# Kernel tuning notes

Measured on AMD Instinct MI355X. Metric: run time of the kernel, lower is better.

## Reference

```python
import jax, jax.numpy as jnp
import numpy as np

VOCAB = 32000
EMBED = 512
HID = 1024          # bi-LSTM summary dim; each direction HID//2
HDIM = 1024         # snli_h_dim
B, T = 128, 128
EPS = 1e-6


def setup_inputs() -> dict:
    key = jax.random.key(0)
    ks = jax.random.split(key, 10)
    Hh = HID // 2
    def rn(k, shape, scale):
        return jax.random.normal(k, shape, jnp.float32) * scale
    embed = rn(ks[0], (VOCAB, EMBED), 0.1).at[0].set(0.0)  # padding_idx=0 row zeroed
    return {
        'hyp_tokens': jax.random.randint(ks[1], (B, T), 0, VOCAB),
        'prem_tokens': jax.random.randint(ks[2], (B, T), 0, VOCAB),
        'embed': embed,
        'W_ih': rn(ks[3], (4 * Hh, EMBED), 1.0 / np.sqrt(Hh)),
        'W_hh': rn(ks[4], (4 * Hh, Hh), 1.0 / np.sqrt(Hh)),
        'b_ih': jnp.zeros((4 * Hh,), jnp.float32),
        'b_hh': jnp.zeros((4 * Hh,), jnp.float32),
        'mlp1_W': rn(ks[5], (HDIM, 4 * HID), np.sqrt(2.0 / (4 * HID))),  # He init
        'mlp1_b': jnp.zeros((HDIM,), jnp.float32),
        'mlp2_W': rn(ks[6], (HDIM, HDIM), np.sqrt(2.0 / HDIM)),
        'mlp2_b': jnp.zeros((HDIM,), jnp.float32),
        'out_W': rn(ks[7], (3, HDIM), np.sqrt(2.0 / HDIM)),
        'out_b': jnp.zeros((3,), jnp.float32),
        'ln0_g': jnp.ones((4 * HID,), jnp.float32), 'ln0_b': jnp.zeros((4 * HID,), jnp.float32),
        'ln1_g': jnp.ones((HDIM,), jnp.float32), 'ln1_b': jnp.zeros((HDIM,), jnp.float32),
        'ln2_g': jnp.ones((HDIM,), jnp.float32), 'ln2_b': jnp.zeros((HDIM,), jnp.float32),
    }


def _lstm_final(x_tbe, W_ih, W_hh, b_ih, b_hh):
    # Runs an LSTM over time (leading axis), returns final (h, c).
    Bn = x_tbe.shape[1]
    Hh = W_hh.shape[1]
    # Precompute input projection for all timesteps: [T, B, 4*Hh]
    xg = jnp.einsum('tbe,ge->tbg', x_tbe, W_ih) + b_ih + b_hh
    def step(carry, xg_t):
        h, c = carry
        gates = xg_t + h @ W_hh.T
        i, f, g, o = jnp.split(gates, 4, axis=-1)  # PyTorch gate order i,f,g,o
        c2 = jax.nn.sigmoid(f) * c + jax.nn.sigmoid(i) * jnp.tanh(g)
        h2 = jax.nn.sigmoid(o) * jnp.tanh(c2)
        return (h2, c2), None
    init = (jnp.zeros((Bn, Hh), x_tbe.dtype), jnp.zeros((Bn, Hh), x_tbe.dtype))
    (h, c), _ = jax.lax.scan(step, init, xg)
    return h, c


def _encode_sent(x, W_ih, W_hh, b_ih, b_hh):
    # Matches encode_sent: same LSTM weights run forward and backward over time;
    # summary = concat(last forward state, last backward state).
    xt = jnp.swapaxes(x, 0, 1)  # [T, B, E]
    hf, cf = _lstm_final(xt, W_ih, W_hh, b_ih, b_hh)
    hb, cb = _lstm_final(xt[::-1], W_ih, W_hh, b_ih, b_hh)
    return jnp.concatenate([hf, hb], axis=-1), jnp.concatenate([cf, cb], axis=-1)


def _ln(x, g, b):
    m = jnp.mean(x, axis=-1, keepdims=True)
    v = jnp.var(x, axis=-1, keepdims=True)
    return (x - m) * jax.lax.rsqrt(v + EPS) * g + b


def reference(hyp_tokens, prem_tokens, embed, W_ih, W_hh, b_ih, b_hh,
              mlp1_W, mlp1_b, mlp2_W, mlp2_b, out_W, out_b,
              ln0_g, ln0_b, ln1_g, ln1_b, ln2_g, ln2_b):
    hyp_e = embed[hyp_tokens]    # [B, T, E]
    prem_e = embed[prem_tokens]
    hyp_h, _ = _encode_sent(hyp_e, W_ih, W_hh, b_ih, b_hh)    # [B, HID]
    prem_h, _ = _encode_sent(prem_e, W_ih, W_hh, b_ih, b_hh)
    # prepare_features: [hyp, prem, prem - hyp, hyp * prem]
    f = jnp.concatenate([hyp_h, prem_h, prem_h - hyp_h, hyp_h * prem_h], axis=-1)
    f = _ln(f, ln0_g, ln0_b)
    f = jax.nn.relu(f @ mlp1_W.T + mlp1_b)
    f = _ln(f, ln1_g, ln1_b)
    f = jax.nn.relu(f @ mlp2_W.T + mlp2_b)
    f = _ln(f, ln2_g, ln2_b)
    return f @ out_W.T + out_b  # [B, 3] logits
```

## Files before the change

kernel.cpp:

```cpp
#include <hip/hip_runtime.h>
#include <hip/hip_bf16.h>

typedef __hip_bfloat16 bf16;
typedef __attribute__((ext_vector_type(8))) short short8;
typedef __attribute__((ext_vector_type(4))) short s16x4;
typedef __attribute__((ext_vector_type(4))) float f32x4;
typedef __attribute__((ext_vector_type(2))) float f32x2;

#define TB 128
#define TT 128
#define EMB 512
#define HH 512
#define G4 2048
#define NROWS 512
#define F4 4096
#define HD 1024

__device__ __forceinline__ bf16 f2bf(float x){ return __float2bfloat16(x); }
__device__ __forceinline__ float bf2f(bf16 x){ return __bfloat162float(x); }

__device__ __forceinline__ float fsigm(float x){
    return __builtin_amdgcn_rcpf(1.f + __builtin_amdgcn_exp2f(-1.44269504089f * x));
}
__device__ __forceinline__ float ftanh(float x){
    float t = __builtin_amdgcn_exp2f(2.88539008178f * x);
    return 1.f - 2.f * __builtin_amdgcn_rcpf(t + 1.f);
}

__device__ __forceinline__ short8 pack8(float4 a, float4 b){
    short8 r;
    r[0] = (short)__bfloat16_as_ushort(f2bf(a.x));
    r[1] = (short)__bfloat16_as_ushort(f2bf(a.y));
    r[2] = (short)__bfloat16_as_ushort(f2bf(a.z));
    r[3] = (short)__bfloat16_as_ushort(f2bf(a.w));
    r[4] = (short)__bfloat16_as_ushort(f2bf(b.x));
    r[5] = (short)__bfloat16_as_ushort(f2bf(b.y));
    r[6] = (short)__bfloat16_as_ushort(f2bf(b.z));
    r[7] = (short)__bfloat16_as_ushort(f2bf(b.w));
    return r;
}

__global__ __launch_bounds__(256) void k_cvt(const float* __restrict__ src,
                                             bf16* __restrict__ dst, int n4)
{
    for (int i = blockIdx.x * 256 + threadIdx.x; i < n4; i += gridDim.x * 256) {
        float4 v = reinterpret_cast<const float4*>(src)[i];
        s16x4 o;
        o[0] = (short)__bfloat16_as_ushort(f2bf(v.x));
        o[1] = (short)__bfloat16_as_ushort(f2bf(v.y));
        o[2] = (short)__bfloat16_as_ushort(f2bf(v.z));
        o[3] = (short)__bfloat16_as_ushort(f2bf(v.w));
        reinterpret_cast<s16x4*>(dst)[i] = o;
    }
}

__global__ __launch_bounds__(256) void k_gather(
    const int* __restrict__ tok_h, const int* __restrict__ tok_p,
    const float* __restrict__ embed, bf16* __restrict__ x_bf)
{
    const int total4 = 2 * TT * TB * (EMB / 4);
    for (int g = blockIdx.x * 256 + threadIdx.x; g < total4; g += gridDim.x * 256) {
        int e4 = g & (EMB / 4 - 1);
        int b  = (g >> 7) & 127;
        int t  = (g >> 14) & 127;
        int s  = g >> 21;
        int tok = (s ? tok_p : tok_h)[b * TT + t];
        float4 v = reinterpret_cast<const float4*>(embed + (size_t)tok * EMB)[e4];
        s16x4 o;
        o[0] = (short)__bfloat16_as_ushort(f2bf(v.x));
        o[1] = (short)__bfloat16_as_ushort(f2bf(v.y));
        o[2] = (short)__bfloat16_as_ushort(f2bf(v.z));
        o[3] = (short)__bfloat16_as_ushort(f2bf(v.w));
        reinterpret_cast<s16x4*>(x_bf + (((size_t)s * TT + t) * TB + b) * EMB)[e4] = o;
    }
}

__global__ __launch_bounds__(256) void k_xproj2(
    const int* __restrict__ tok_h, const int* __restrict__ tok_p,
    const float* __restrict__ embed, const bf16* __restrict__ W_ihb,
    const float* __restrict__ b_ih, const float* __restrict__ b_hh,
    bf16* __restrict__ xg)
{
    __shared__ __align__(16) short As[64][512];
    const int mb = blockIdx.x;
    const int nb = blockIdx.y;
    const int tid = threadIdx.x;
    const int w = tid >> 6, lane = tid & 63, l16 = lane & 15, kq = lane >> 4;
    const int m0 = mb * 64;
    const int s  = m0 >> 14;
    const int tt = (m0 >> 7) & 127;
    const int bbase = m0 & 127;
    const int* tp = s ? tok_p : tok_h;

#pragma unroll
    for (int it = 0; it < 16; ++it) {
        int idx = it * 256 + tid;
        int row = idx >> 6;
        int ch  = idx & 63;
        int tok = tp[(bbase + row) * TT + tt];
        const float* er = embed + (size_t)tok * EMB + ch * 8;
        float4 v0 = *(const float4*)er;
        float4 v1 = *(const float4*)(er + 4);
        *(short8*)&As[row][(ch ^ (row & 7)) * 8] = pack8(v0, v1);
    }
    __syncthreads();

    const int c0 = nb * 256 + w * 64;
    f32x4 acc[4][4];
#pragma unroll
    for (int mt = 0; mt < 4; ++mt)
#pragma unroll
        for (int nt = 0; nt < 4; ++nt) acc[mt][nt] = (f32x4)0.f;

    for (int kk = 0; kk < 16; ++kk) {
        short8 bfr[4];
#pragma unroll
        for (int nt = 0; nt < 4; ++nt)
            bfr[nt] = *(const short8*)(W_ihb + (size_t)(c0 + nt * 16 + l16) * EMB + kk * 32 + kq * 8);
#pragma unroll
        for (int mt = 0; mt < 4; ++mt) {
            int row = mt * 16 + l16;
            short8 a = *(const short8*)&As[row][(((kk * 4 + kq) ^ (row & 7)) * 8)];
#pragma unroll
            for (int nt = 0; nt < 4; ++nt)
                acc[mt][nt] = __builtin_amdgcn_mfma_f32_16x16x32_bf16(a, bfr[nt], acc[mt][nt], 0, 0, 0);
        }
    }
#pragma unroll
    for (int nt = 0; nt < 4; ++nt) {
        int col = c0 + nt * 16 + l16;
        float bias = b_ih[col] + b_hh[col];
#pragma unroll
        for (int mt = 0; mt < 4; ++mt)
#pragma unroll
            for (int q = 0; q < 4; ++q) {
                int m = m0 + mt * 16 + kq * 4 + q;
                xg[(size_t)m * G4 + col] = f2bf(acc[mt][nt][q] + bias);
            }
    }
}

__global__ __launch_bounds__(512, 1) void k_persist8(
    const bf16* __restrict__ xg, const float* __restrict__ W_hh,
    const float* __restrict__ b_ih, const float* __restrict__ b_hh,
    float* __restrict__ h_f32, float* __restrict__ h_fin,
    int* __restrict__ slots, int* __restrict__ xinfo)
{
    __shared__ __align__(16) short hstage[2][16][512];
    __shared__ float ga[16][16][18];

    const int tid = threadIdx.x;
    const int bid = blockIdx.x;
    const int rg = bid & 31;
    const int cb = bid >> 5;
    const int w = tid >> 6, lane = tid & 63, l16 = lane & 15, kq = lane >> 4;
    const int j0 = cb * 64;
    const int r0 = rg * 16;
    const int run = rg >> 3;
    const int s = run >> 1, dirb = run & 1;
    const int b0 = (rg & 7) * 16;

    bool mall = false;
    {
        int myx;
        asm volatile("s_getreg_b32 %0, hwreg(HW_REG_XCC_ID)" : "=s"(myx));
        if (tid == 0)
            __hip_atomic_store(&xinfo[bid], (myx & 15) + 1,
                               __ATOMIC_RELAXED, __HIP_MEMORY_SCOPE_AGENT);
        int v0 = 0;
        for (int c = 0; c < 8; ++c) {
            int v;
            do {
                v = __hip_atomic_load(&xinfo[c * 32 + rg],
                                      __ATOMIC_RELAXED, __HIP_MEMORY_SCOPE_AGENT);
                if (!v) __builtin_amdgcn_s_sleep(2);
            } while (!v);
            if (c == 0) v0 = v;
            else if (v != v0) mall = true;
        }
    }

    short8 Bf[2][16];
#pragma unroll
    for (int nt = 0; nt < 2; ++nt) {
        int n = 2 * w + nt;
        int gcol = (n >> 2) * HH + j0 + (n & 3) * 16 + l16;
        const float* wr = W_hh + (size_t)gcol * HH;
#pragma unroll
        for (int kk = 0; kk < 16; ++kk) {
            float4 v0 = *(const float4*)(wr + kk * 32 + kq * 8);
            float4 v1 = *(const float4*)(wr + kk * 32 + kq * 8 + 4);
            Bf[nt][kk] = pack8(v0, v1);
        }
    }

    const int urow = tid >> 5;
    const int jseg = tid & 31;
    float bsum[2][4];
#pragma unroll
    for (int e = 0; e < 2; ++e)
#pragma unroll
        for (int g = 0; g < 4; ++g) {
            int j = g * HH + j0 + jseg * 2 + e;
            bsum[e][g] = b_ih[j] + b_hh[j];
        }
    float creg[2] = {0.f, 0.f};
    const size_t HSF = (size_t)NROWS * HH;

    int rowoff[8];
#pragma unroll
    for (int nt = 0; nt < 2; ++nt) {
        int n = 2 * w + nt;
        int gcol = (n >> 2) * HH + j0 + (n & 3) * 16 + l16;
#pragma unroll
        for (int q = 0; q < 4; ++q)
            rowoff[nt * 4 + q] = (b0 + kq * 4 + q) * G4 + gcol;
    }

    unsigned xp[8];
    {
        int te0 = dirb ? (TT - 1) : 0;
        const bf16* xr = xg + ((size_t)(s * TT + te0) * TB) * G4;
#pragma unroll
        for (int i = 0; i < 8; ++i)
            xp[i] = (unsigned)__bfloat16_as_ushort(xr[rowoff[i]]);
    }

    for (int t = 0; t < TT; ++t) {
        const int p = t & 1;

        f32x4 hv[4];
        {
            unsigned long long a = (unsigned long long)(
                h_f32 + (size_t)p * HSF + (size_t)(r0 + urow) * HH + jseg * 16);
            if (mall) {
#pragma unroll
                for (int i = 0; i < 4; ++i)
                    asm volatile("global_load_dwordx4 %0, %1, off sc0 sc1"
                                 : "=v"(hv[i]) : "v"(a + i * 16));
            } else {
#pragma unroll
                for (int i = 0; i < 4; ++i)
                    asm volatile("global_load_dwordx4 %0, %1, off sc0"
                                 : "=v"(hv[i]) : "v"(a + i * 16));
            }
        }
        asm volatile("s_waitcnt vmcnt(0)" ::: "memory");
        __builtin_amdgcn_sched_barrier(0);

#pragma unroll
        for (int half = 0; half < 2; ++half) {
            short8 hi, lo;
#pragma unroll
            for (int i2 = 0; i2 < 8; ++i2) {
                float v = hv[half * 2 + (i2 >> 2)][i2 & 3];
                bf16 hb = f2bf(v);
                hi[i2] = (short)__bfloat16_as_ushort(hb);
                lo[i2] = (short)__bfloat16_as_ushort(f2bf(v - bf2f(hb)));
            }
            int ch = (2 * jseg + half) ^ (urow & 7);
            *(short8*)&hstage[0][urow][ch * 8] = hi;
            *(short8*)&hstage[1][urow][ch * 8] = lo;
        }

        f32x4 acc[2];
#pragma unroll
        for (int nt = 0; nt < 2; ++nt)
#pragma unroll
            for (int q = 0; q < 4; ++q)
                acc[nt][q] = __uint_as_float(xp[nt * 4 + q] << 16);

        __syncthreads();

#pragma unroll
        for (int kk = 0; kk < 16; ++kk) {
            int ch = ((kk * 4 + kq) ^ (l16 & 7)) * 8;
            short8 ahi = *(const short8*)&hstage[0][l16][ch];
            short8 alo = *(const short8*)&hstage[1][l16][ch];
#pragma unroll
            for (int nt = 0; nt < 2; ++nt) {
                acc[nt] = __builtin_amdgcn_mfma_f32_16x16x32_bf16(alo, Bf[nt][kk], acc[nt], 0, 0, 0);
                acc[nt] = __builtin_amdgcn_mfma_f32_16x16x32_bf16(ahi, Bf[nt][kk], acc[nt], 0, 0, 0);
            }
        }

#pragma unroll
        for (int nt = 0; nt < 2; ++nt)
#pragma unroll
            for (int q = 0; q < 4; ++q)
                ga[2 * w + nt][kq * 4 + q][l16] = acc[nt][q];
        __syncthreads();

        float hn2[2];
#pragma unroll
        for (int e = 0; e < 2; ++e) {
            int jc = jseg * 2 + e;
            int sub = jc >> 4, c15 = jc & 15;
            float pi = ga[0 + sub][urow][c15]  + bsum[e][0];
            float pf = ga[4 + sub][urow][c15]  + bsum[e][1];
            float pg = ga[8 + sub][urow][c15]  + bsum[e][2];
            float po = ga[12 + sub][urow][c15] + bsum[e][3];
            float cn = fsigm(pf) * creg[e] + fsigm(pi) * ftanh(pg);
            float hn = fsigm(po) * ftanh(cn);
            creg[e] = cn;
            hn2[e] = hn;
        }
        {
            unsigned long long a = (unsigned long long)(
                h_f32 + (size_t)(p ^ 1) * HSF + (size_t)(r0 + urow) * HH + j0 + jseg * 2);
            f32x2 val; val[0] = hn2[0]; val[1] = hn2[1];
            if (mall)
                asm volatile("global_store_dwordx2 %0, %1, off sc0 sc1"
                             :: "v"(a), "v"(val) : "memory");
            else
                asm volatile("global_store_dwordx2 %0, %1, off sc0"
                             :: "v"(a), "v"(val) : "memory");
        }
        if (t == TT - 1) {
            size_t fb = (size_t)(r0 + urow) * HH + j0 + jseg * 2;
            h_fin[fb] = hn2[0];
            h_fin[fb + 1] = hn2[1];
            break;
        }

        {
            int ten = dirb ? (TT - 2 - t) : (t + 1);
            const bf16* xrn = xg + ((size_t)(s * TT + ten) * TB) * G4;
#pragma unroll
            for (int i = 0; i < 8; ++i)
                asm volatile("global_load_ushort %0, %1, off"
                             : "=v"(xp[i])
                             : "v"((unsigned long long)(xrn + rowoff[i])));
        }
        asm volatile("s_waitcnt vmcnt(8)" ::: "memory");
        __syncthreads();
        if (tid == 0)
            __hip_atomic_store(&slots[rg * 8 + cb], t + 1,
                               __ATOMIC_RELAXED, __HIP_MEMORY_SCOPE_AGENT);
        {
            int sidx = rg * 8 + (lane & 7);
            while (true) {
                int v = (lane < 8)
                    ? __hip_atomic_load(&slots[sidx],
                                        __ATOMIC_RELAXED, __HIP_MEMORY_SCOPE_AGENT)
                    : 0x7fffffff;
                if (__all(v >= t + 1)) break;
                __builtin_amdgcn_s_sleep(1);
            }
        }
    }
}

__global__ __launch_bounds__(256) void k_persist(
    const bf16* __restrict__ x_bf,
    const float* __restrict__ W_ih, const float* __restrict__ W_hh,
    const float* __restrict__ b_ih, const float* __restrict__ b_hh,
    bf16* __restrict__ h_hi, bf16* __restrict__ h_lo,
    float* __restrict__ h_fin, int* slots)
{
    __shared__ short Wl[4 * 16 * 16 * 64];
    __shared__ float ga[4][64][17];

    const int tid = threadIdx.x;
    const int bx  = blockIdx.x;
    const int mi  = bx & 7;
    const int cj  = bx >> 3;
    const int w    = tid >> 6;
    const int lane = tid & 63;
    const int l16 = lane & 15;
    const int kq  = lane >> 4;
    const int j0  = cj * 16;
    const int r0  = mi * 64;
    const int run = mi >> 1;
    const int s   = run >> 1;
    const int dirb = run & 1;

    {
        int gc  = tid >> 2;
        int g   = gc >> 4, c = gc & 15;
        int kq4 = tid & 3;
        const float* wxr = W_ih + (size_t)(g * HH + j0 + c) * EMB;
        const float* whr = W_hh + (size_t)(g * HH + j0 + c) * HH;
        for (int kb = 0; kb < 16; ++kb) {
            int k  = kq4 * 128 + kb * 8;
            int kk = k >> 5;
            int eq = (k >> 3) & 3;
            float4 x0 = *(const float4*)(wxr + k);
            float4 x1 = *(const float4*)(wxr + k + 4);
            float4 h0 = *(const float4*)(whr + k);
            float4 h1 = *(const float4*)(whr + k + 4);
            int base = ((g * 16 + kk) * 16 + c) * 64;
            int sx = eq ^ (c & 7);
            int sh = (eq + 4) ^ (c & 7);
            *(short8*)&Wl[base + sx * 8] = pack8(x0, x1);
            *(short8*)&Wl[base + sh * 8] = pack8(h0, h1);
        }
    }

    float bsum[4];
    {
        int j = j0 + (tid & 15);
#pragma unroll
        for (int g = 0; g < 4; ++g) bsum[g] = b_ih[g * HH + j] + b_hh[g * HH + j];
    }
    float creg[4] = {0.f, 0.f, 0.f, 0.f};
    __syncthreads();

    const size_t HS = (size_t)NROWS * HH;
    for (int t = 0; t < TT; ++t) {
        const int p  = t & 1;
        const int te = dirb ? (TT - 1 - t) : t;
        const bf16* hb = h_hi + (size_t)p * HS;
        const bf16* lb = h_lo + (size_t)p * HS;
        const bf16* xr0 = x_bf + ((size_t)(s * TT + te) * TB) * EMB;

        f32x4 acc[4];
#pragma unroll
        for (int mt = 0; mt < 4; ++mt) acc[mt] = (f32x4)0.f;

        const bf16 *ph[4], *pl[4], *px[4];
#pragma unroll
        for (int mt = 0; mt < 4; ++mt) {
            int r = r0 + mt * 16 + l16;
            ph[mt] = hb + (size_t)r * HH;
            pl[mt] = lb + (size_t)r * HH;
            px[mt] = xr0 + (size_t)(r & 127) * EMB;
        }

        for (int kk = 0; kk < 16; ++kk) {
            int cbse = ((w * 16 + kk) * 16 + l16) * 64;
            short8 fx = *(const short8*)&Wl[cbse + ((kq ^ (lane & 7)) * 8)];
            short8 fh = *(const short8*)&Wl[cbse + (((kq + 4) ^ (lane & 7)) * 8)];
            int k0 = kk * 32 + kq * 8;
#pragma unroll
            for (int mt = 0; mt < 4; ++mt) {
                short8 ax  = *(const short8*)(px[mt] + k0);
                short8 ahi = *(const short8*)(ph[mt] + k0);
                short8 alo = *(const short8*)(pl[mt] + k0);
                acc[mt] = __builtin_amdgcn_mfma_f32_16x16x32_bf16(ax,  fx, acc[mt], 0, 0, 0);
                acc[mt] = __builtin_amdgcn_mfma_f32_16x16x32_bf16(alo, fh, acc[mt], 0, 0, 0);
                acc[mt] = __builtin_amdgcn_mfma_f32_16x16x32_bf16(ahi, fh, acc[mt], 0, 0, 0);
            }
        }
#pragma unroll
        for (int mt = 0; mt < 4; ++mt)
#pragma unroll
            for (int q = 0; q < 4; ++q)
                ga[w][mt * 16 + kq * 4 + q][l16] = acc[mt][q];
        __syncthreads();

        bf16* hob = h_hi + (size_t)(p ^ 1) * HS;
        bf16* lob = h_lo + (size_t)(p ^ 1) * HS;
        const int colc = tid & 15;
        const int j = j0 + colc;
#pragma unroll
        for (int q = 0; q < 4; ++q) {
            int rl = (tid >> 4) + q * 16;
            int r  = r0 + rl;
            float pi = ga[0][rl][colc] + bsum[0];
            float pf = ga[1][rl][colc] + bsum[1];
            float pg = ga[2][rl][colc] + bsum[2];
            float po = ga[3][rl][colc] + bsum[3];
            float si = 1.f / (1.f + expf(-pi));
            float sf = 1.f / (1.f + expf(-pf));
            float so = 1.f / (1.f + expf(-po));
            float tg = tanhf(pg);
            float cn = sf * creg[q] + si * tg;
            float hn = so * tanhf(cn);
            creg[q] = cn;
            size_t idx = (size_t)r * HH + j;
            bf16 hi = f2bf(hn);
            hob[idx] = hi;
            lob[idx] = f2bf(hn - bf2f(hi));
            if (t == TT - 1) h_fin[idx] = hn;
        }
        if (t == TT - 1) break;

        __syncthreads();
        if (tid == 0)
            __hip_atomic_store(&slots[mi * 32 + cj], t + 1,
                               __ATOMIC_RELEASE, __HIP_MEMORY_SCOPE_AGENT);
        if (tid < 64) {
            const int tgt = t + 1;
            while (true) {
                int v = (lane < 32)
                    ? __hip_atomic_load(&slots[mi * 32 + lane],
                                        __ATOMIC_RELAXED, __HIP_MEMORY_SCOPE_AGENT)
                    : tgt;
                if (__all(v >= tgt)) break;
                __builtin_amdgcn_s_sleep(1);
            }
            __builtin_amdgcn_fence(__ATOMIC_ACQUIRE, "agent");
        }
        __syncthreads();
    }
}

template<int GATH>
__global__ __launch_bounds__(256) void k_step(
    const bf16* __restrict__ x_bf, const float* __restrict__ embed,
    const int* __restrict__ tok_h, const int* __restrict__ tok_p,
    const bf16* __restrict__ W_ihb, const bf16* __restrict__ W_hhb,
    const float* __restrict__ b_ih, const float* __restrict__ b_hh,
    const bf16* __restrict__ h_hi_in, const bf16* __restrict__ h_lo_in,
    bf16* __restrict__ h_hi_out, bf16* __restrict__ h_lo_out,
    float* __restrict__ c_buf, float* __restrict__ h_fin, int t)
{
    __shared__ float lds[4][64][17];

    const int blk = blockIdx.x;
    const int mi = blk >> 5;
    const int ji = blk & 31;
    const int w    = threadIdx.x >> 6;
    const int lane = threadIdx.x & 63;
    const int l16 = lane & 15;
    const int kq  = lane >> 4;

    const int run = mi >> 1;
    const int s   = run >> 1;
    const int te  = (run & 1) ? (TT - 1 - t) : t;
    const int r0  = mi * 64;

    const bf16*  hhp[4];
    const bf16*  hlp[4];
    const bf16*  xbp[4];
    const float* xfp[4];
#pragma unroll
    for (int mt = 0; mt < 4; ++mt) {
        int r = r0 + mt * 16 + l16;
        hhp[mt] = h_hi_in + (size_t)r * HH;
        hlp[mt] = h_lo_in + (size_t)r * HH;
        int b = r & 127;
        if (GATH) {
            xbp[mt] = x_bf + (((size_t)s * TT + te) * TB + b) * EMB;
        } else {
            int tok = (s ? tok_p : tok_h)[b * TT + te];
            xfp[mt] = embed + (size_t)tok * EMB;
        }
    }

    const int gcol = w * HH + ji * 16 + l16;
    const bf16* wh = W_hhb + (size_t)gcol * HH;
    const bf16* wx = W_ihb + (size_t)gcol * EMB;

    f32x4 acc[4];
#pragma unroll
    for (int mt = 0; mt < 4; ++mt) acc[mt] = (f32x4)0.f;

    for (int kk = 0; kk < HH / 32; ++kk) {
        const int k0 = kk * 32 + kq * 8;
        short8 bwh = *reinterpret_cast<const short8*>(wh + k0);
        short8 bwx = *reinterpret_cast<const short8*>(wx + k0);
#pragma unroll
        for (int mt = 0; mt < 4; ++mt) {
            short8 ax;
            if (GATH) {
                ax = *reinterpret_cast<const short8*>(xbp[mt] + k0);
            } else {
                float4 v0 = *reinterpret_cast<const float4*>(xfp[mt] + k0);
                float4 v1 = *reinterpret_cast<const float4*>(xfp[mt] + k0 + 4);
                ax = pack8(v0, v1);
            }
            short8 ahi = *reinterpret_cast<const short8*>(hhp[mt] + k0);
            short8 alo = *reinterpret_cast<const short8*>(hlp[mt] + k0);
            acc[mt] = __builtin_amdgcn_mfma_f32_16x16x32_bf16(ax,  bwx, acc[mt], 0, 0, 0);
            acc[mt] = __builtin_amdgcn_mfma_f32_16x16x32_bf16(alo, bwh, acc[mt], 0, 0, 0);
            acc[mt] = __builtin_amdgcn_mfma_f32_16x16x32_bf16(ahi, bwh, acc[mt], 0, 0, 0);
        }
    }
#pragma unroll
    for (int mt = 0; mt < 4; ++mt)
#pragma unroll
        for (int q = 0; q < 4; ++q)
            lds[w][mt * 16 + kq * 4 + q][l16] = acc[mt][q];
    __syncthreads();

    const int tid = threadIdx.x;
#pragma unroll
    for (int q = 0; q < 4; ++q) {
        int cell = tid + q * 256;
        int rl  = cell >> 4;
        int col = cell & 15;
        int r = r0 + rl;
        int j = ji * 16 + col;

        float pi = lds[0][rl][col] + b_ih[j]          + b_hh[j];
        float pf = lds[1][rl][col] + b_ih[HH + j]     + b_hh[HH + j];
        float pg = lds[2][rl][col] + b_ih[2 * HH + j] + b_hh[2 * HH + j];
        float po = lds[3][rl][col] + b_ih[3 * HH + j] + b_hh[3 * HH + j];

        float si = 1.f / (1.f + expf(-pi));
        float sf = 1.f / (1.f + expf(-pf));
        float so = 1.f / (1.f + expf(-po));
        float tg = tanhf(pg);

        size_t idx = (size_t)r * HH + j;
        float cn = sf * c_buf[idx] + si * tg;
        float hn = so * tanhf(cn);
        c_buf[idx] = cn;

        bf16 hi = f2bf(hn);
        h_hi_out[idx] = hi;
        h_lo_out[idx] = f2bf(hn - bf2f(hi));
        if (t == TT - 1) h_fin[idx] = hn;
    }
}

__global__ __launch_bounds__(256) void k_feat_ln0(
    const float* __restrict__ h_fin, const float* __restrict__ g,
    const float* __restrict__ be, bf16* __restrict__ f_out)
{
    const int b = blockIdx.x;
    const int tid = threadIdx.x;
    float v[16];
    float s = 0.f, sq = 0.f;
#pragma unroll
    for (int i = 0; i < 16; ++i) {
        int e = i * 256 + tid;
        int region = e >> 10;
        int idx = e & 1023;
        int runh = (idx < 512) ? 0 : 1;
        int jj = idx & 511;
        float hy = h_fin[((size_t)(runh * TB + b)) * HH + jj];
        float pr = h_fin[((size_t)((runh + 2) * TB + b)) * HH + jj];
        float val = (region == 0) ? hy : (region == 1) ? pr
                  : (region == 2) ? (pr - hy) : (hy * pr);
        v[i] = val;
        s += val;
        sq += val * val;
    }
    __shared__ float shs[4], shq[4];
    for (int o = 32; o; o >>= 1) { s += __shfl_down(s, o); sq += __shfl_down(sq, o); }
    int w = tid >> 6, lane = tid & 63;
    if (!lane) { shs[w] = s; shq[w] = sq; }
    __syncthreads();
    s  = shs[0] + shs[1] + shs[2] + shs[3];
    sq = shq[0] + shq[1] + shq[2] + shq[3];
    float mean = s / (float)F4;
    float var  = sq / (float)F4 - mean * mean;
    float rstd = rsqrtf(var + 1e-6f);
#pragma unroll
    for (int i = 0; i < 16; ++i) {
        int e = i * 256 + tid;
        float nv = (v[i] - mean) * rstd * g[e] + be[e];
        f_out[(size_t)b * F4 + e] = f2bf(nv);
    }
}

template<int KTOT, int NCH>
__global__ __launch_bounds__(256) void k_mlp_sk(
    const bf16* __restrict__ A, const float* __restrict__ Bw,
    float* __restrict__ part)
{
    const int KC = KTOT / NCH;
    const int nb = blockIdx.x, mb = blockIdx.y, kc = blockIdx.z;
    const int w    = threadIdx.x >> 6;
    const int lane = threadIdx.x & 63;
    const int wr = w >> 1, wc = w & 1;
    const int l16 = lane & 15;
    const int kq  = lane >> 4;
    const int m0 = mb * 64 + wr * 32;
    const int c0 = nb * 64 + wc * 32;

    f32x4 acc[2][2];
#pragma unroll
    for (int i = 0; i < 2; ++i)
#pragma unroll
        for (int j = 0; j < 2; ++j) acc[i][j] = (f32x4)0.f;

    for (int kk = kc * (KC / 32); kk < (kc + 1) * (KC / 32); ++kk) {
        const int k0 = kk * 32 + kq * 8;
        short8 a[2], bb[2];
#pragma unroll
        for (int i = 0; i < 2; ++i)
            a[i] = *reinterpret_cast<const short8*>(A + (size_t)(m0 + i * 16 + l16) * KTOT + k0);
#pragma unroll
        for (int j = 0; j < 2; ++j) {
            const float* bp = Bw + (size_t)(c0 + j * 16 + l16) * KTOT + k0;
            float4 v0 = *reinterpret_cast<const float4*>(bp);
            float4 v1 = *reinterpret_cast<const float4*>(bp + 4);
            bb[j] = pack8(v0, v1);
        }
#pragma unroll
        for (int i = 0; i < 2; ++i)
#pragma unroll
            for (int j = 0; j < 2; ++j)
                acc[i][j] = __builtin_amdgcn_mfma_f32_16x16x32_bf16(a[i], bb[j], acc[i][j], 0, 0, 0);
    }
#pragma unroll
    for (int i = 0; i < 2; ++i)
#pragma unroll
        for (int j = 0; j < 2; ++j) {
            int gg = c0 + j * 16 + l16;
#pragma unroll
            for (int q = 0; q < 4; ++q) {
                int m = m0 + i * 16 + kq * 4 + q;
                part[((size_t)kc * TB + m) * HD + gg] = acc[i][j][q];
            }
        }
}

template<int NCH>
__global__ __launch_bounds__(256) void k_redln(
    const float* __restrict__ part, const float* __restrict__ bias,
    const float* __restrict__ g, const float* __restrict__ be,
    bf16* __restrict__ out)
{
    const int b = blockIdx.x;
    const int tid = threadIdx.x;
    float v[4];
    float s = 0.f, sq = 0.f;
#pragma unroll
    for (int i = 0; i < 4; ++i) {
        int e = i * 256 + tid;
        float val = bias[e];
#pragma unroll
        for (int c = 0; c < NCH; ++c) val += part[((size_t)c * TB + b) * HD + e];
        val = fmaxf(val, 0.f);
        v[i] = val; s += val; sq += val * val;
    }
    __shared__ float shs[4], shq[4];
    for (int o = 32; o; o >>= 1) { s += __shfl_down(s, o); sq += __shfl_down(sq, o); }
    int w = tid >> 6, lane = tid & 63;
    if (!lane) { shs[w] = s; shq[w] = sq; }
    __syncthreads();
    s  = shs[0] + shs[1] + shs[2] + shs[3];
    sq = shq[0] + shq[1] + shq[2] + shq[3];
    float mean = s / (float)HD;
    float var  = sq / (float)HD - mean * mean;
    float rstd = rsqrtf(var + 1e-6f);
#pragma unroll
    for (int i = 0; i < 4; ++i) {
        int e = i * 256 + tid;
        out[(size_t)b * HD + e] = f2bf((v[i] - mean) * rstd * g[e] + be[e]);
    }
}

template<int NCH>
__global__ __launch_bounds__(256) void k_redln_out(
    const float* __restrict__ part, const float* __restrict__ bias,
    const float* __restrict__ g, const float* __restrict__ be,
    const float* __restrict__ Wt, const float* __restrict__ ob,
    float* __restrict__ out)
{
    const int b = blockIdx.x;
    const int tid = threadIdx.x;
    float v[4];
    float s = 0.f, sq = 0.f;
#pragma unroll
    for (int i = 0; i < 4; ++i) {
        int e = i * 256 + tid;
        float val = bias[e];
#pragma unroll
        for (int c = 0; c < NCH; ++c) val += part[((size_t)c * TB + b) * HD + e];
        val = fmaxf(val, 0.f);
        v[i] = val; s += val; sq += val * val;
    }
    __shared__ float shs[4], shq[4];
    for (int o = 32; o; o >>= 1) { s += __shfl_down(s, o); sq += __shfl_down(sq, o); }
    int w = tid >> 6, lane = tid & 63;
    if (!lane) { shs[w] = s; shq[w] = sq; }
    __syncthreads();
    s  = shs[0] + shs[1] + shs[2] + shs[3];
    sq = shq[0] + shq[1] + shq[2] + shq[3];
    float mean = s / (float)HD;
    float var  = sq / (float)HD - mean * mean;
    float rstd = rsqrtf(var + 1e-6f);
    float p0 = 0.f, p1 = 0.f, p2 = 0.f;
#pragma unroll
    for (int i = 0; i < 4; ++i) {
        int e = i * 256 + tid;
        float f = (v[i] - mean) * rstd * g[e] + be[e];
        p0 += f * Wt[e];
        p1 += f * Wt[HD + e];
        p2 += f * Wt[2 * HD + e];
    }
    for (int o = 32; o; o >>= 1) {
        p0 += __shfl_down(p0, o);
        p1 += __shfl_down(p1, o);
        p2 += __shfl_down(p2, o);
    }
    __shared__ float sh[4][3];
    if (!lane) { sh[w][0] = p0; sh[w][1] = p1; sh[w][2] = p2; }
    __syncthreads();
    if (tid < 3)
        out[b * 3 + tid] = sh[0][tid] + sh[1][tid] + sh[2][tid] + sh[3][tid] + ob[tid];
}

extern "C" void kernel_launch(void* const* d_in, const int* in_sizes, int n_in,
                              void* d_out, int out_size, void* d_ws, size_t ws_size,
                              hipStream_t stream)
{
    const int*   tok_h  = (const int*)  d_in[0];
    const int*   tok_p  = (const int*)  d_in[1];
    const float* embed  = (const float*)d_in[2];
    const float* W_ih   = (const float*)d_in[3];
    const float* W_hh   = (const float*)d_in[4];
    const float* b_ih   = (const float*)d_in[5];
    const float* b_hh   = (const float*)d_in[6];
    const float* mlp1_W = (const float*)d_in[7];
    const float* mlp1_b = (const float*)d_in[8];
    const float* mlp2_W = (const float*)d_in[9];
    const float* mlp2_b = (const float*)d_in[10];
    const float* out_W  = (const float*)d_in[11];
    const float* out_b  = (const float*)d_in[12];
    const float* ln0_g  = (const float*)d_in[13];
    const float* ln0_b  = (const float*)d_in[14];
    const float* ln1_g  = (const float*)d_in[15];
    const float* ln1_b  = (const float*)d_in[16];
    const float* ln2_g  = (const float*)d_in[17];
    const float* ln2_b  = (const float*)d_in[18];

    char* ws = (char*)d_ws;
    size_t off = 0;
    bf16*  f_ln0 = (bf16*)(ws + off);  off += (size_t)TB * F4 * 2;
    float* part  = (float*)(ws + off); off += (size_t)8 * TB * HD * 4;
    bf16*  f_ln1 = (bf16*)(ws + off);  off += (size_t)TB * HD * 2;
    float* h_fin = (float*)(ws + off); off += (size_t)NROWS * HH * 4;
    bf16*  h_hi  = (bf16*)(ws + off);  off += (size_t)2 * NROWS * HH * 2;
    bf16*  h_lo  = (bf16*)(ws + off);  off += (size_t)2 * NROWS * HH * 2;
    int*   slots = (int*)(ws + off);   off += 4096;
    float* c_buf = (float*)(ws + off); off += (size_t)NROWS * HH * 4;
    bf16*  W_ihb = (bf16*)(ws + off);  off += (size_t)G4 * EMB * 2;
    bf16*  W_hhb = (bf16*)(ws + off);  off += (size_t)G4 * HH * 2;
    float* h_f32 = (float*)h_hi;
    int*   xinfo = slots + 256;
    bf16*  xg   = (bf16*)(ws + off);
    bf16*  x_bf = (bf16*)(ws + off);
    const size_t need_primary = off + (size_t)2 * TT * TB * G4 * 2;
    const size_t need_f1      = off + (size_t)2 * TT * TB * EMB * 2;

    (void)hipMemsetAsync(h_hi, 0, (size_t)4 * NROWS * HH * 2 + 4096, stream);

    const size_t HS = (size_t)NROWS * HH;
    if (ws_size >= need_primary) {
        k_cvt<<<512, 256, 0, stream>>>(W_ih, W_ihb, G4 * EMB / 4);
        k_xproj2<<<dim3(512, 8), 256, 0, stream>>>(tok_h, tok_p, embed, W_ihb,
                                                   b_ih, b_hh, xg);
        void* args[] = {(void*)&xg, (void*)&W_hh, (void*)&b_ih, (void*)&b_hh,
                        (void*)&h_f32, (void*)&h_fin, (void*)&slots, (void*)&xinfo};
        (void)hipLaunchCooperativeKernel((void*)k_persist8, dim3(256), dim3(512),
                                         args, 0, stream);
    } else if (ws_size >= need_f1) {
        k_gather<<<4096, 256, 0, stream>>>(tok_h, tok_p, embed, x_bf);
        void* args[] = {(void*)&x_bf, (void*)&W_ih, (void*)&W_hh,
                        (void*)&b_ih, (void*)&b_hh,
                        (void*)&h_hi, (void*)&h_lo, (void*)&h_fin, (void*)&slots};
        (void)hipLaunchCooperativeKernel((void*)k_persist, dim3(256), dim3(256),
                                         args, 0, stream);
    } else {
        (void)hipMemsetAsync(c_buf, 0, (size_t)NROWS * HH * 4, stream);
        k_cvt<<<512, 256, 0, stream>>>(W_ih, W_ihb, G4 * EMB / 4);
        k_cvt<<<512, 256, 0, stream>>>(W_hh, W_hhb, G4 * HH / 4);
        for (int t = 0; t < TT; ++t) {
            int p = t & 1;
            k_step<0><<<256, 256, 0, stream>>>(x_bf, embed, tok_h, tok_p,
                W_ihb, W_hhb, b_ih, b_hh,
                h_hi + (size_t)p * HS, h_lo + (size_t)p * HS,
                h_hi + (size_t)(p ^ 1) * HS, h_lo + (size_t)(p ^ 1) * HS,
                c_buf, h_fin, t);
        }
    }

    k_feat_ln0<<<TB, 256, 0, stream>>>(h_fin, ln0_g, ln0_b, f_ln0);
    k_mlp_sk<F4, 8><<<dim3(16, 2, 8), 256, 0, stream>>>(f_ln0, mlp1_W, part);
    k_redln<8><<<TB, 256, 0, stream>>>(part, mlp1_b, ln1_g, ln1_b, f_ln1);
    k_mlp_sk<HD, 4><<<dim3(16, 2, 4), 256, 0, stream>>>(f_ln1, mlp2_W, part);
    k_redln_out<4><<<TB, 256, 0, stream>>>(part, mlp2_b, ln2_g, ln2_b,
                                           out_W, out_b, (float*)d_out);
}
```

Measured before the change: 702.7 us.

## Store input-projection gates in per-lane slab layout for vector loads in recurrence

The input-projection kernel now writes its bf16 gate outputs in a slab layout matched to each lane of the persistent LSTM kernel. Each lane can then prefetch its next-timestep gates with a single 16-byte load instead of eight scattered 2-byte loads. The sync slot stride is widened to 32 ints so different row groups' flags sit on separate cache lines, and xinfo moves to its own region. This costs more complex index math and ties the producer's layout to the consumer's tiling.

New measurement: 659.7 us. 6.1% less time.

```diff
diff --git a/kernel.cpp b/kernel.cpp
--- a/kernel.cpp
+++ b/kernel.cpp
@@ -15,6 +15,7 @@
 #define NROWS 512
 #define F4 4096
 #define HD 1024
+#define SLABW 32768
 
 __device__ __forceinline__ bf16 f2bf(float x){ return __float2bfloat16(x); }
 __device__ __forceinline__ float bf2f(bf16 x){ return __bfloat162float(x); }
@@ -75,7 +76,7 @@
     }
 }
 
-__global__ __launch_bounds__(256) void k_xproj2(
+__global__ __launch_bounds__(256) void k_xproj3(
     const int* __restrict__ tok_h, const int* __restrict__ tok_p,
     const float* __restrict__ embed, const bf16* __restrict__ W_ihb,
     const float* __restrict__ b_ih, const float* __restrict__ b_hh,
@@ -126,21 +127,34 @@
                 acc[mt][nt] = __builtin_amdgcn_mfma_f32_16x16x32_bf16(a, bfr[nt], acc[mt][nt], 0, 0, 0);
         }
     }
-#pragma unroll
-    for (int nt = 0; nt < 4; ++nt) {
-        int col = c0 + nt * 16 + l16;
-        float bias = b_ih[col] + b_hh[col];
-#pragma unroll
-        for (int mt = 0; mt < 4; ++mt)
-#pragma unroll
-            for (int q = 0; q < 4; ++q) {
-                int m = m0 + mt * 16 + kq * 4 + q;
-                xg[(size_t)m * G4 + col] = f2bf(acc[mt][nt][q] + bias);
+
+    const int gate = nb >> 1;
+    const int cbp  = (nb & 1) * 4 + w;
+    const size_t slab = ((size_t)s * TT + tt) * SLABW;
+    const int lanew = kq * 16 + l16;
+#pragma unroll
+    for (int mt = 0; mt < 4; ++mt) {
+        int B1 = (bbase >> 4) + mt;
+#pragma unroll
+        for (int mh = 0; mh < 2; ++mh) {
+            int wc = gate * 2 + mh;
+            size_t word = slab + (((size_t)(B1 * 8 + cbp) * 8 + wc) * 64 + lanew);
+            short8 o;
+#pragma unroll
+            for (int nt = 0; nt < 2; ++nt) {
+                int nt4 = mh * 2 + nt;
+                int colx = nb * 256 + w * 64 + nt4 * 16 + l16;
+                float bias = b_ih[colx] + b_hh[colx];
+#pragma unroll
+                for (int q = 0; q < 4; ++q)
+                    o[nt * 4 + q] = (short)__bfloat16_as_ushort(f2bf(acc[mt][nt4][q] + bias));
             }
-    }
-}
-
-__global__ __launch_bounds__(512, 1) void k_persist8(
+            *(short8*)(xg + word * 8) = o;
+        }
+    }
+}
+
+__global__ __launch_bounds__(512, 1) void k_persist10(
     const bf16* __restrict__ xg, const float* __restrict__ W_hh,
     const float* __restrict__ b_ih, const float* __restrict__ b_hh,
     float* __restrict__ h_f32, float* __restrict__ h_fin,
@@ -158,7 +172,6 @@
     const int r0 = rg * 16;
     const int run = rg >> 3;
     const int s = run >> 1, dirb = run & 1;
-    const int b0 = (rg & 7) * 16;
 
     bool mall = false;
     {
@@ -207,23 +220,13 @@
     float creg[2] = {0.f, 0.f};
     const size_t HSF = (size_t)NROWS * HH;
 
-    int rowoff[8];
-#pragma unroll
-    for (int nt = 0; nt < 2; ++nt) {
-        int n = 2 * w + nt;
-        int gcol = (n >> 2) * HH + j0 + (n & 3) * 16 + l16;
-#pragma unroll
-        for (int q = 0; q < 4; ++q)
-            rowoff[nt * 4 + q] = (b0 + kq * 4 + q) * G4 + gcol;
-    }
-
-    unsigned xp[8];
+    const size_t woff = (((size_t)(rg & 7) * 8 + cb) * 8 + w) * 64 + lane;
+
+    short8 xp;
     {
         int te0 = dirb ? (TT - 1) : 0;
-        const bf16* xr = xg + ((size_t)(s * TT + te0) * TB) * G4;
-#pragma unroll
-        for (int i = 0; i < 8; ++i)
-            xp[i] = (unsigned)__bfloat16_as_ushort(xr[rowoff[i]]);
+        xp = *(const short8*)((const char*)xg +
+                              (((size_t)(s * TT + te0)) * SLABW + woff) * 16);
     }
 
     for (int t = 0; t < TT; ++t) {
@@ -268,7 +271,8 @@
         for (int nt = 0; nt < 2; ++nt)
 #pragma unroll
             for (int q = 0; q < 4; ++q)
-                acc[nt][q] = __uint_as_float(xp[nt * 4 + q] << 16);
+                acc[nt][q] = __uint_as_float(
+                    ((unsigned)(unsigned short)xp[nt * 4 + q]) << 16);
 
         __syncthreads();
 
@@ -325,20 +329,18 @@
 
         {
             int ten = dirb ? (TT - 2 - t) : (t + 1);
-            const bf16* xrn = xg + ((size_t)(s * TT + ten) * TB) * G4;
-#pragma unroll
-            for (int i = 0; i < 8; ++i)
-                asm volatile("global_load_ushort %0, %1, off"
-                             : "=v"(xp[i])
-                             : "v"((unsigned long long)(xrn + rowoff[i])));
-        }
-        asm volatile("s_waitcnt vmcnt(8)" ::: "memory");
+            unsigned long long xa = (unsigned long long)xg +
+                (((size_t)(s * TT + ten)) * SLABW + woff) * 16;
+            asm volatile("global_load_dwordx4 %0, %1, off"
+                         : "=v"(xp) : "v"(xa));
+        }
+        asm volatile("s_waitcnt vmcnt(1)" ::: "memory");
         __syncthreads();
         if (tid == 0)
-            __hip_atomic_store(&slots[rg * 8 + cb], t + 1,
+            __hip_atomic_store(&slots[rg * 32 + cb], t + 1,
                                __ATOMIC_RELAXED, __HIP_MEMORY_SCOPE_AGENT);
         {
-            int sidx = rg * 8 + (lane & 7);
+            int sidx = rg * 32 + (lane & 7);
             while (true) {
                 int v = (lane < 8)
                     ? __hip_atomic_load(&slots[sidx],
@@ -820,26 +822,26 @@
     bf16*  h_hi  = (bf16*)(ws + off);  off += (size_t)2 * NROWS * HH * 2;
     bf16*  h_lo  = (bf16*)(ws + off);  off += (size_t)2 * NROWS * HH * 2;
     int*   slots = (int*)(ws + off);   off += 4096;
+    int*   xinfo = (int*)(ws + off);   off += 4096;
     float* c_buf = (float*)(ws + off); off += (size_t)NROWS * HH * 4;
     bf16*  W_ihb = (bf16*)(ws + off);  off += (size_t)G4 * EMB * 2;
     bf16*  W_hhb = (bf16*)(ws + off);  off += (size_t)G4 * HH * 2;
     float* h_f32 = (float*)h_hi;
-    int*   xinfo = slots + 256;
     bf16*  xg   = (bf16*)(ws + off);
     bf16*  x_bf = (bf16*)(ws + off);
     const size_t need_primary = off + (size_t)2 * TT * TB * G4 * 2;
     const size_t need_f1      = off + (size_t)2 * TT * TB * EMB * 2;
 
-    (void)hipMemsetAsync(h_hi, 0, (size_t)4 * NROWS * HH * 2 + 4096, stream);
+    (void)hipMemsetAsync(h_hi, 0, (size_t)4 * NROWS * HH * 2 + 8192, stream);
 
     const size_t HS = (size_t)NROWS * HH;
     if (ws_size >= need_primary) {
         k_cvt<<<512, 256, 0, stream>>>(W_ih, W_ihb, G4 * EMB / 4);
-        k_xproj2<<<dim3(512, 8), 256, 0, stream>>>(tok_h, tok_p, embed, W_ihb,
+        k_xproj3<<<dim3(512, 8), 256, 0, stream>>>(tok_h, tok_p, embed, W_ihb,
                                                    b_ih, b_hh, xg);
         void* args[] = {(void*)&xg, (void*)&W_hh, (void*)&b_ih, (void*)&b_hh,
                         (void*)&h_f32, (void*)&h_fin, (void*)&slots, (void*)&xinfo};
-        (void)hipLaunchCooperativeKernel((void*)k_persist8, dim3(256), dim3(512),
+        (void)hipLaunchCooperativeKernel((void*)k_persist10, dim3(256), dim3(512),
                                          args, 0, stream);
     } else if (ws_size >= need_f1) {
         k_gather<<<4096, 256, 0, stream>>>(tok_h, tok_p, embed, x_bf);
```
